# Kernel optimization log

Hardware: AMD Instinct MI355X
Metric: run time of the kernel (lower is better)

## Reference

```python
import jax, jax.numpy as jnp
import numpy as np
from jax import lax

KH, KW, K = 3, 3, 9
PAD, BN_EPS = 1, 1e-5


def setup_inputs() -> dict:
    key = jax.random.key(0)
    ks = jax.random.split(key, 10)
    B, CHI, CHO, H, W = 2, 64, 64, 128, 128
    x = jax.random.normal(ks[0], (B, CHI, H, W), dtype=jnp.float32)
    # offset/mask branch conv: 3*K output channels (o1, o2, mask)
    w_off = jax.random.normal(ks[1], (3 * K, CHI, KH, KW), dtype=jnp.float32) * 0.01
    b_off = jax.random.normal(ks[2], (3 * K,), dtype=jnp.float32) * 0.01
    # main deformable conv weight/bias
    fan = CHI * K
    weight = jax.random.normal(ks[3], (CHO, CHI, KH, KW), dtype=jnp.float32) / np.sqrt(fan)
    bias = jax.random.normal(ks[4], (CHO,), dtype=jnp.float32) * 0.01
    # BatchNorm (eval-mode) params
    gamma = jax.random.uniform(ks[5], (CHO,), minval=0.5, maxval=1.5, dtype=jnp.float32)
    beta = jax.random.normal(ks[6], (CHO,), dtype=jnp.float32) * 0.1
    run_mean = jax.random.normal(ks[7], (CHO,), dtype=jnp.float32) * 0.1
    run_var = jax.random.uniform(ks[8], (CHO,), minval=0.5, maxval=1.5, dtype=jnp.float32)
    return {"x": x, "w_off": w_off, "b_off": b_off, "weight": weight,
            "bias": bias, "gamma": gamma, "beta": beta,
            "run_mean": run_mean, "run_var": run_var}


def _dcn_bn_relu(x, w_off, b_off, weight, bias, gamma, beta, run_mean, run_var):
    B, C, H, W = x.shape
    CHO = weight.shape[0]
    # offset/mask branch: regular 3x3 conv, stride 1, pad 1
    om = lax.conv_general_dilated(
        x, w_off, window_strides=(1, 1), padding=[(PAD, PAD), (PAD, PAD)],
        dimension_numbers=("NCHW", "OIHW", "NCHW")) + b_off[None, :, None, None]
    o1, o2, m = jnp.split(om, 3, axis=1)          # each [B, K, H, W]
    offset = jnp.concatenate([o1, o2], axis=1)    # [B, 2K, H, W]
    off_y = offset[:, 0::2]                       # interleaved (y, x) per tap, as in DCNv2 CUDA
    off_x = offset[:, 1::2]
    mask = jax.nn.sigmoid(m)                      # [B, K, H, W] modulation

    # sampling positions: p = p0 + p_k + offset
    ky, kx = jnp.meshgrid(jnp.arange(KH), jnp.arange(KW), indexing="ij")
    ky = ky.reshape(K).astype(x.dtype)
    kx = kx.reshape(K).astype(x.dtype)
    hh = jnp.arange(H, dtype=x.dtype)
    ww = jnp.arange(W, dtype=x.dtype)
    py = hh[None, None, :, None] - PAD + ky[None, :, None, None] + off_y  # [B,K,H,W]
    px = ww[None, None, None, :] - PAD + kx[None, :, None, None] + off_x

    y0f = jnp.floor(py)
    x0f = jnp.floor(px)
    ly = (py - y0f)[..., None]
    lx = (px - x0f)[..., None]
    y0 = y0f.astype(jnp.int32)
    x0 = x0f.astype(jnp.int32)
    bidx = jnp.arange(B)[:, None, None, None]

    def gather(yi, xi):
        valid = ((yi >= 0) & (yi < H) & (xi >= 0) & (xi < W)).astype(x.dtype)
        yc = jnp.clip(yi, 0, H - 1)
        xc = jnp.clip(xi, 0, W - 1)
        g = x[bidx, :, yc, xc]                    # [B, K, H, W, C]
        return g * valid[..., None]

    v00 = gather(y0, x0)
    v01 = gather(y0, x0 + 1)
    v10 = gather(y0 + 1, x0)
    v11 = gather(y0 + 1, x0 + 1)
    sampled = (v00 * (1 - ly) * (1 - lx) + v01 * (1 - ly) * lx
               + v10 * ly * (1 - lx) + v11 * ly * lx)
    sampled = sampled * mask[..., None]           # modulated

    out = jnp.einsum("bkhwc,ock->bohw", sampled,
                     weight.reshape(CHO, C, K)) + bias[None, :, None, None]

    # eval-mode BatchNorm + ReLU
    inv = gamma / jnp.sqrt(run_var + BN_EPS)
    out = (out - run_mean[None, :, None, None]) * inv[None, :, None, None] \
          + beta[None, :, None, None]
    return jax.nn.relu(out)


def reference(x, w_off, b_off, weight, bias, gamma, beta, run_mean, run_var):
    return _dcn_bn_relu(x, w_off, b_off, weight, bias, gamma, beta, run_mean, run_var)
```

## Files before the change

### kernel.cpp

```cpp
#include <hip/hip_runtime.h>
#include <hip/hip_bf16.h>

#define HH 128
#define WW 128
#define CI 64
#define CO 64
#define SLS 584
#define HPS 72
#define HALW 18

typedef __attribute__((ext_vector_type(8))) short short8;
typedef __attribute__((ext_vector_type(4))) float floatx4;

__device__ __forceinline__ unsigned short f2bf(float f) {
  union { float f; unsigned u; } uu; uu.f = f;
  unsigned r = uu.u + 0x7FFFu + ((uu.u >> 16) & 1u);
  return (unsigned short)(r >> 16);
}
__device__ __forceinline__ unsigned pack2bf(float lo, float hi) {
  return (unsigned)f2bf(lo) | ((unsigned)f2bf(hi) << 16);
}
__device__ __forceinline__ float bfl(unsigned u) { return __uint_as_float(u << 16); }
__device__ __forceinline__ float bfh(unsigned u) { return __uint_as_float(u & 0xffff0000u); }

__global__ __launch_bounds__(256) void prep_kernel(
    const float* __restrict__ x, unsigned* __restrict__ xTb_u,
    const float* __restrict__ weight, const float* __restrict__ bias,
    const float* __restrict__ gamma, const float* __restrict__ beta,
    const float* __restrict__ mean, const float* __restrict__ var,
    const float* __restrict__ w_off, const float* __restrict__ b_off,
    unsigned short* __restrict__ Wm, unsigned short* __restrict__ w2,
    float* __restrict__ bias2, float* __restrict__ boff2) {
  __shared__ unsigned T2[128 * 33];
  int bid = blockIdx.x;
  int tid = threadIdx.x;
  if (bid < 256) {
    int b = bid >> 7, h = bid & 127;
    int cp = tid >> 3, wc = tid & 7;
    const float* xp = x + (((long)(b * CI + 2 * cp) * HH + h) * WW + wc * 16);
#pragma unroll
    for (int i = 0; i < 4; i++) {
      float4 a0 = *(const float4*)(xp + i * 4);
      float4 a1 = *(const float4*)(xp + HH * WW + i * 4);
      T2[(wc * 16 + i * 4 + 0) * 33 + cp] = pack2bf(a0.x, a1.x);
      T2[(wc * 16 + i * 4 + 1) * 33 + cp] = pack2bf(a0.y, a1.y);
      T2[(wc * 16 + i * 4 + 2) * 33 + cp] = pack2bf(a0.z, a1.z);
      T2[(wc * 16 + i * 4 + 3) * 33 + cp] = pack2bf(a0.w, a1.w);
    }
    __syncthreads();
    int px = tid >> 1, g = tid & 1;
    const unsigned* src = &T2[px * 33 + g * 16];
    unsigned* dst = xTb_u + (long)(bid * 128 + px) * 32 + g * 16;
#pragma unroll
    for (int q = 0; q < 4; q++)
      *(uint4*)(dst + 4 * q) =
          make_uint4(src[4 * q], src[4 * q + 1], src[4 * q + 2], src[4 * q + 3]);
    return;
  }
  int idx = (bid - 256) * 256 + tid;
  if (idx < 32) boff2[idx] = (idx < 27) ? b_off[idx] : 0.f;
  if (idx >= CO * 576) return;
  int o = idx / 576, kc = idx - o * 576;
  int k = kc >> 6, c = kc & 63;
  float inv = gamma[o] * rsqrtf(var[o] + 1e-5f);
  Wm[idx] = f2bf(weight[(o * CI + c) * 9 + k] * inv);
  if (kc == 0) bias2[o] = (bias[o] - mean[o]) * inv + beta[o];
  if (o < 27) w2[idx] = f2bf(w_off[o * 576 + c * 9 + k]);
  else if (o < 32) w2[idx] = 0;
}

__global__ __launch_bounds__(256) void dcn_kernel(
    const unsigned short* __restrict__ xTb,
    const unsigned short* __restrict__ w2, const float* __restrict__ boff2,
    const unsigned short* __restrict__ Wm, const float* __restrict__ bias2,
    float* __restrict__ out) {
  __shared__ char smem[26752];
  short* hal = (short*)smem;
  __hip_bfloat16* SL = (__hip_bfloat16*)smem;
  float* omL = (float*)(smem + 18688);
  float4* Pw = (float4*)(smem + 23296);
  int2* Po = (int2*)(smem + 25600);

  int bid = blockIdx.x;
  int s = bid & 7;
  int n = bid >> 3;
  int b = n >> 7;
  int rem = n & 127;
  int h = s * 16 + (rem >> 3);
  int w0 = (rem & 7) * 16;
  int tid = threadIdx.x, lane = tid & 63, wave = tid >> 6;

#pragma unroll
  for (int it = 0; it < 2; it++) {
    int t = it * 256 + tid;
    if (t < 432) {
      int row = t / 144;
      int r2 = t - row * 144;
      int xi = r2 >> 3, cg = r2 & 7;
      int y = h - 1 + row, xx = w0 - 1 + xi;
      uint4 v = make_uint4(0u, 0u, 0u, 0u);
      if ((unsigned)y < (unsigned)HH && (unsigned)xx < (unsigned)WW)
        v = *(const uint4*)(xTb + (long)((b * HH + y) * WW + xx) * CI + cg * 8);
      *(uint4*)(hal + (row * HALW + xi) * HPS + cg * 8) = v;
    }
  }
  __syncthreads();

  {
    int r16 = lane & 15, quad = lane >> 4;
    int m16 = wave & 1, kh = wave >> 1;
    floatx4 t = {0.f, 0.f, 0.f, 0.f};
    if (kh == 0) t = *(const floatx4*)(boff2 + m16 * 16 + quad * 4);
    const short* ap = (const short*)(w2 + (m16 * 16 + r16) * 576 + kh * 32 + quad * 8);
#pragma unroll
    for (int kk = 0; kk < 9; kk++) {
      int dy = kk / 3, dxk = kk - 3 * (kk / 3);
      short8 bfrag = *(const short8*)(hal + (dy * HALW + r16 + dxk) * HPS + kh * 32 + quad * 8);
      short8 afrag = *(const short8*)(ap + kk * 64);
      t = __builtin_amdgcn_mfma_f32_16x16x32_bf16(afrag, bfrag, t, 0, 0, 0);
    }
    *(floatx4*)(omL + kh * 576 + r16 * 36 + m16 * 16 + quad * 4) = t;
  }
  __syncthreads();

  if (lane < 36) {
    int p_loc = (lane * 7282) >> 16;
    int k = lane - p_loc * 9;
    int p = wave * 4 + p_loc;
    const float* o0 = omL + p * 36;
    const float* o1 = omL + 576 + p * 36;
    float oy = o0[2 * k] + o1[2 * k];
    float ox = o0[2 * k + 1] + o1[2 * k + 1];
    float mm = o0[18 + k] + o1[18 + k];
    float msk = 1.f / (1.f + __expf(-mm));
    int ky = (k * 11) >> 5;
    int kx = k - 3 * ky;
    float py = (float)(h - 1 + ky) + oy;
    float pxx = (float)(w0 + p - 1 + kx) + ox;
    float y0f = floorf(py), x0f = floorf(pxx);
    float ly = py - y0f, lx = pxx - x0f;
    int y0 = (int)y0f, x0 = (int)x0f;
    int y1 = y0 + 1, x1 = x0 + 1;
    float lylx = ly * lx;
    bool y0v = (unsigned)y0 < (unsigned)HH, y1v = (unsigned)y1 < (unsigned)HH;
    bool x0v = (unsigned)x0 < (unsigned)WW, x1v = (unsigned)x1 < (unsigned)WW;
    int yc0 = min(max(y0, 0), HH - 1), yc1 = min(max(y1, 0), HH - 1);
    int xc0 = min(max(x0, 0), WW - 1), xc1 = min(max(x1, 0), WW - 1);
    Pw[p * 9 + k] = make_float4((y0v && x0v) ? (1.f - ly - lx + lylx) * msk : 0.f,
                                (y0v && x1v) ? (lx - lylx) * msk : 0.f,
                                (y1v && x0v) ? (ly - lylx) * msk : 0.f,
                                (y1v && x1v) ? lylx * msk : 0.f);
    int dxs = (xc1 - xc0) * CI;
    int dys = (yc1 - yc0) * WW * CI;
    Po[p * 9 + k] = make_int2((yc0 * WW + xc0) * CI, dxs | (dys << 16));
  }

  {
    int cq = lane & 15, pl = lane >> 4;
    int p = wave * 4 + pl;
    const unsigned short* xb = xTb + (long)b * (HH * WW * CI);
#pragma unroll
    for (int k = 0; k < 9; k++) {
      float4 wv = Pw[p * 9 + k];
      int2 po = Po[p * 9 + k];
      int o00 = po.x + cq * 4;
      int dx = po.y & 0xffff;
      int dyv = po.y >> 16;
      uint2 u00 = *(const uint2*)(xb + o00);
      uint2 u01 = *(const uint2*)(xb + o00 + dx);
      uint2 u10 = *(const uint2*)(xb + o00 + dyv);
      uint2 u11 = *(const uint2*)(xb + o00 + dyv + dx);
      float lo0 = bfl(u00.x) * wv.x + bfl(u01.x) * wv.y + bfl(u10.x) * wv.z + bfl(u11.x) * wv.w;
      float hi0 = bfh(u00.x) * wv.x + bfh(u01.x) * wv.y + bfh(u10.x) * wv.z + bfh(u11.x) * wv.w;
      float lo1 = bfl(u00.y) * wv.x + bfl(u01.y) * wv.y + bfl(u10.y) * wv.z + bfl(u11.y) * wv.w;
      float hi1 = bfh(u00.y) * wv.x + bfh(u01.y) * wv.y + bfh(u10.y) * wv.z + bfh(u11.y) * wv.w;
      *(uint2*)(&SL[p * SLS + k * 64 + cq * 4]) =
          make_uint2(pack2bf(lo0, hi0), pack2bf(lo1, hi1));
    }
  }
  __syncthreads();

  {
    int r16 = lane & 15, quad = lane >> 4;
    floatx4 acc = *(const floatx4*)(bias2 + wave * 16 + quad * 4);
    const unsigned short* Ap = Wm + (wave * 16 + r16) * 576 + quad * 8;
    const __hip_bfloat16* Sp = &SL[r16 * SLS + quad * 8];
#pragma unroll
    for (int kc0 = 0; kc0 < 576; kc0 += 32) {
      short8 av = *(const short8*)(Ap + kc0);
      short8 bv = *(const short8*)(Sp + kc0);
      acc = __builtin_amdgcn_mfma_f32_16x16x32_bf16(av, bv, acc, 0, 0, 0);
    }
#pragma unroll
    for (int r = 0; r < 4; r++) {
      int o = wave * 16 + quad * 4 + r;
      out[((b * CO + o) * HH + h) * WW + w0 + r16] = fmaxf(acc[r], 0.f);
    }
  }
}

extern "C" void kernel_launch(void* const* d_in, const int* in_sizes, int n_in,
                              void* d_out, int out_size, void* d_ws, size_t ws_size,
                              hipStream_t stream) {
  const float* x = (const float*)d_in[0];
  const float* w_off = (const float*)d_in[1];
  const float* b_off = (const float*)d_in[2];
  const float* weight = (const float*)d_in[3];
  const float* bias = (const float*)d_in[4];
  const float* gamma = (const float*)d_in[5];
  const float* beta = (const float*)d_in[6];
  const float* run_mean = (const float*)d_in[7];
  const float* run_var = (const float*)d_in[8];
  float* outp = (float*)d_out;

  char* ws = (char*)d_ws;
  unsigned* xTb = (unsigned*)ws;
  unsigned short* Wm = (unsigned short*)(ws + 4194304);
  unsigned short* w2 = (unsigned short*)(ws + 4268032);
  float* bias2 = (float*)(ws + 4304896);
  float* boff2 = (float*)(ws + 4305152);

  prep_kernel<<<400, 256, 0, stream>>>(x, xTb, weight, bias, gamma, beta,
                                       run_mean, run_var, w_off, b_off,
                                       Wm, w2, bias2, boff2);
  dcn_kernel<<<2048, 256, 0, stream>>>((const unsigned short*)xTb, w2, boff2,
                                       Wm, bias2, outp);
}
```

Baseline: 117.1 us.

## Split prep transpose into more blocks, batch gathers, dual MFMA accumulators

The prep transpose now splits each row into four 32-pixel chunks across 1024 blocks, which raises parallelism and shrinks shared memory. In the DCN kernel, all 36 bilinear gather loads are issued before any arithmetic so their memory latency overlaps. Both MFMA loops alternate between two accumulators to break the serial dependency chain, and launch bounds now request 4 blocks per CU. The batched gathers add register pressure, which may conflict with the occupancy hint and cause spilling.

```diff
diff --git a/kernel.cpp b/kernel.cpp
--- a/kernel.cpp
+++ b/kernel.cpp
@@ -31,33 +31,27 @@
     const float* __restrict__ w_off, const float* __restrict__ b_off,
     unsigned short* __restrict__ Wm, unsigned short* __restrict__ w2,
     float* __restrict__ bias2, float* __restrict__ boff2) {
-  __shared__ unsigned T2[128 * 33];
+  __shared__ unsigned T2[32 * 33];
   int bid = blockIdx.x;
   int tid = threadIdx.x;
-  if (bid < 256) {
-    int b = bid >> 7, h = bid & 127;
+  if (bid < 1024) {
+    int b = bid >> 9, h = (bid >> 2) & 127, q = bid & 3;
     int cp = tid >> 3, wc = tid & 7;
-    const float* xp = x + (((long)(b * CI + 2 * cp) * HH + h) * WW + wc * 16);
-#pragma unroll
-    for (int i = 0; i < 4; i++) {
-      float4 a0 = *(const float4*)(xp + i * 4);
-      float4 a1 = *(const float4*)(xp + HH * WW + i * 4);
-      T2[(wc * 16 + i * 4 + 0) * 33 + cp] = pack2bf(a0.x, a1.x);
-      T2[(wc * 16 + i * 4 + 1) * 33 + cp] = pack2bf(a0.y, a1.y);
-      T2[(wc * 16 + i * 4 + 2) * 33 + cp] = pack2bf(a0.z, a1.z);
-      T2[(wc * 16 + i * 4 + 3) * 33 + cp] = pack2bf(a0.w, a1.w);
-    }
+    const float* xp = x + (((long)(b * CI + 2 * cp) * HH + h) * WW + q * 32 + wc * 4);
+    float4 a0 = *(const float4*)xp;
+    float4 a1 = *(const float4*)(xp + HH * WW);
+    T2[(wc * 4 + 0) * 33 + cp] = pack2bf(a0.x, a1.x);
+    T2[(wc * 4 + 1) * 33 + cp] = pack2bf(a0.y, a1.y);
+    T2[(wc * 4 + 2) * 33 + cp] = pack2bf(a0.z, a1.z);
+    T2[(wc * 4 + 3) * 33 + cp] = pack2bf(a0.w, a1.w);
     __syncthreads();
-    int px = tid >> 1, g = tid & 1;
-    const unsigned* src = &T2[px * 33 + g * 16];
-    unsigned* dst = xTb_u + (long)(bid * 128 + px) * 32 + g * 16;
-#pragma unroll
-    for (int q = 0; q < 4; q++)
-      *(uint4*)(dst + 4 * q) =
-          make_uint4(src[4 * q], src[4 * q + 1], src[4 * q + 2], src[4 * q + 3]);
+    int px = tid >> 3, g = tid & 7;
+    const unsigned* src = &T2[px * 33 + g * 4];
+    unsigned* dst = xTb_u + ((long)((b * HH + h) * WW + q * 32 + px)) * 32 + g * 4;
+    *(uint4*)dst = make_uint4(src[0], src[1], src[2], src[3]);
     return;
   }
-  int idx = (bid - 256) * 256 + tid;
+  int idx = (bid - 1024) * 256 + tid;
   if (idx < 32) boff2[idx] = (idx < 27) ? b_off[idx] : 0.f;
   if (idx >= CO * 576) return;
   int o = idx / 576, kc = idx - o * 576;
@@ -69,7 +63,7 @@
   else if (o < 32) w2[idx] = 0;
 }
 
-__global__ __launch_bounds__(256) void dcn_kernel(
+__global__ __launch_bounds__(256, 4) void dcn_kernel(
     const unsigned short* __restrict__ xTb,
     const unsigned short* __restrict__ w2, const float* __restrict__ boff2,
     const unsigned short* __restrict__ Wm, const float* __restrict__ bias2,
@@ -109,16 +103,21 @@
   {
     int r16 = lane & 15, quad = lane >> 4;
     int m16 = wave & 1, kh = wave >> 1;
-    floatx4 t = {0.f, 0.f, 0.f, 0.f};
-    if (kh == 0) t = *(const floatx4*)(boff2 + m16 * 16 + quad * 4);
+    floatx4 t0 = {0.f, 0.f, 0.f, 0.f};
+    floatx4 t1 = {0.f, 0.f, 0.f, 0.f};
+    if (kh == 0) t0 = *(const floatx4*)(boff2 + m16 * 16 + quad * 4);
     const short* ap = (const short*)(w2 + (m16 * 16 + r16) * 576 + kh * 32 + quad * 8);
 #pragma unroll
     for (int kk = 0; kk < 9; kk++) {
       int dy = kk / 3, dxk = kk - 3 * (kk / 3);
       short8 bfrag = *(const short8*)(hal + (dy * HALW + r16 + dxk) * HPS + kh * 32 + quad * 8);
       short8 afrag = *(const short8*)(ap + kk * 64);
-      t = __builtin_amdgcn_mfma_f32_16x16x32_bf16(afrag, bfrag, t, 0, 0, 0);
-    }
+      if (kk & 1)
+        t1 = __builtin_amdgcn_mfma_f32_16x16x32_bf16(afrag, bfrag, t1, 0, 0, 0);
+      else
+        t0 = __builtin_amdgcn_mfma_f32_16x16x32_bf16(afrag, bfrag, t0, 0, 0, 0);
+    }
+    floatx4 t = t0 + t1;
     *(floatx4*)(omL + kh * 576 + r16 * 36 + m16 * 16 + quad * 4) = t;
   }
   __syncthreads();
@@ -159,17 +158,22 @@
     int cq = lane & 15, pl = lane >> 4;
     int p = wave * 4 + pl;
     const unsigned short* xb = xTb + (long)b * (HH * WW * CI);
+    uint2 u[9][4];
 #pragma unroll
     for (int k = 0; k < 9; k++) {
-      float4 wv = Pw[p * 9 + k];
       int2 po = Po[p * 9 + k];
       int o00 = po.x + cq * 4;
       int dx = po.y & 0xffff;
       int dyv = po.y >> 16;
-      uint2 u00 = *(const uint2*)(xb + o00);
-      uint2 u01 = *(const uint2*)(xb + o00 + dx);
-      uint2 u10 = *(const uint2*)(xb + o00 + dyv);
-      uint2 u11 = *(const uint2*)(xb + o00 + dyv + dx);
+      u[k][0] = *(const uint2*)(xb + o00);
+      u[k][1] = *(const uint2*)(xb + o00 + dx);
+      u[k][2] = *(const uint2*)(xb + o00 + dyv);
+      u[k][3] = *(const uint2*)(xb + o00 + dyv + dx);
+    }
+#pragma unroll
+    for (int k = 0; k < 9; k++) {
+      float4 wv = Pw[p * 9 + k];
+      uint2 u00 = u[k][0], u01 = u[k][1], u10 = u[k][2], u11 = u[k][3];
       float lo0 = bfl(u00.x) * wv.x + bfl(u01.x) * wv.y + bfl(u10.x) * wv.z + bfl(u11.x) * wv.w;
       float hi0 = bfh(u00.x) * wv.x + bfh(u01.x) * wv.y + bfh(u10.x) * wv.z + bfh(u11.x) * wv.w;
       float lo1 = bfl(u00.y) * wv.x + bfl(u01.y) * wv.y + bfl(u10.y) * wv.z + bfl(u11.y) * wv.w;
@@ -182,15 +186,20 @@
 
   {
     int r16 = lane & 15, quad = lane >> 4;
-    floatx4 acc = *(const floatx4*)(bias2 + wave * 16 + quad * 4);
+    floatx4 acc0 = *(const floatx4*)(bias2 + wave * 16 + quad * 4);
+    floatx4 acc1 = {0.f, 0.f, 0.f, 0.f};
     const unsigned short* Ap = Wm + (wave * 16 + r16) * 576 + quad * 8;
     const __hip_bfloat16* Sp = &SL[r16 * SLS + quad * 8];
 #pragma unroll
-    for (int kc0 = 0; kc0 < 576; kc0 += 32) {
-      short8 av = *(const short8*)(Ap + kc0);
-      short8 bv = *(const short8*)(Sp + kc0);
-      acc = __builtin_amdgcn_mfma_f32_16x16x32_bf16(av, bv, acc, 0, 0, 0);
-    }
+    for (int kc0 = 0; kc0 < 576; kc0 += 64) {
+      short8 av0 = *(const short8*)(Ap + kc0);
+      short8 bv0 = *(const short8*)(Sp + kc0);
+      acc0 = __builtin_amdgcn_mfma_f32_16x16x32_bf16(av0, bv0, acc0, 0, 0, 0);
+      short8 av1 = *(const short8*)(Ap + kc0 + 32);
+      short8 bv1 = *(const short8*)(Sp + kc0 + 32);
+      acc1 = __builtin_amdgcn_mfma_f32_16x16x32_bf16(av1, bv1, acc1, 0, 0, 0);
+    }
+    floatx4 acc = acc0 + acc1;
 #pragma unroll
     for (int r = 0; r < 4; r++) {
       int o = wave * 16 + quad * 4 + r;
@@ -220,9 +229,9 @@
   float* bias2 = (float*)(ws + 4304896);
   float* boff2 = (float*)(ws + 4305152);
 
-  prep_kernel<<<400, 256, 0, stream>>>(x, xTb, weight, bias, gamma, beta,
-                                       run_mean, run_var, w_off, b_off,
-                                       Wm, w2, bias2, boff2);
+  prep_kernel<<<1168, 256, 0, stream>>>(x, xTb, weight, bias, gamma, beta,
+                                        run_mean, run_var, w_off, b_off,
+                                        Wm, w2, bias2, boff2);
   dcn_kernel<<<2048, 256, 0, stream>>>((const unsigned short*)xTb, w2, boff2,
                                        Wm, bias2, outp);
 }
```

New measurement: 112.5 us. -3.9%, faster.
